# Kernel tuning notes

Hardware: AMD Instinct MI355X
Metric: run time of the kernel (lower is better)

The kernel has to match this reference:

```python
import jax, jax.numpy as jnp
import numpy as np

B, T, C, K, V = 4, 2048, 1024, 1024, 1024
SQRT_K = float(np.sqrt(K))


def setup_inputs() -> dict:
    key = jax.random.key(0)
    ks = jax.random.split(key, 7)
    s = 0.02
    return {
        "x": jax.random.normal(ks[0], (B, T, C), jnp.float32),
        "Wq": (jax.random.normal(ks[1], (C, K), jnp.float32) * s),
        "bq": jnp.zeros((K,), jnp.float32),
        "Wk": (jax.random.normal(ks[2], (C, K), jnp.float32) * s),
        "bk": jnp.zeros((K,), jnp.float32),
        "Wv": (jax.random.normal(ks[3], (C, V), jnp.float32) * s),
        "bv": jnp.zeros((V,), jnp.float32),
    }


def reference(x, Wq, bq, Wk, bk, Wv, bv):
    # projections: [B,T,C] @ [C,K] -> [B,T,K]
    q = x @ Wq + bq
    k = x @ Wk + bk
    v = x @ Wv + bv
    # logits[b,t,s] = q[b,t,:] . k[b,s,:]
    logits = jnp.einsum("btk,bsk->bts", q, k)
    # original mask: mask[j,i] = 1 if i > j -> strict upper triangle masked to -inf
    seq = logits.shape[1]
    mask = jnp.triu(jnp.ones((seq, seq), bool), k=1)
    logits = jnp.where(mask[None, :, :], -jnp.inf, logits)
    # NOTE: original softmax is over dim=1 (query axis), not the key axis
    probs = jax.nn.softmax(logits / SQRT_K, axis=1)
    read = jnp.einsum("bts,bsv->btv", probs, v)
    return jnp.concatenate((x, read), axis=2)
```

## Files before the change

### kernel.cpp

```cpp
#include <hip/hip_runtime.h>
#include <hip/hip_bf16.h>
#include <stdint.h>

#define DEVI __device__ __forceinline__

using u16 = unsigned short;
typedef __attribute__((ext_vector_type(8))) _Float16 halfx8;
typedef __attribute__((ext_vector_type(8))) unsigned short u16x8;
typedef __attribute__((ext_vector_type(4))) float f32x4;

constexpr int BB = 4, TT = 2048, CC = 1024, KD = 1024, VD = 1024;
constexpr int QKVW = 3072;
constexpr int OUTW = CC + VD;
constexpr float INV_SQRT_K = 0.03125f;

DEVI u16 f2h(float f) {
  _Float16 h = (_Float16)f;
  return __builtin_bit_cast(u16, h);
}
DEVI float h2f(u16 u) {
  return (float)__builtin_bit_cast(_Float16, u);
}

DEVI void gload16(const u16* g, u16* l) {
  __builtin_amdgcn_global_load_lds(
      (const __attribute__((address_space(1))) void*)g,
      (__attribute__((address_space(3))) void*)l, 16, 0, 0);
}

__global__ void cast_x_copy(const float* __restrict__ x, u16* __restrict__ xh,
                            float* __restrict__ out) {
  size_t i = (size_t)blockIdx.x * blockDim.x + threadIdx.x;
  float4 v = reinterpret_cast<const float4*>(x)[i];
  ushort4 u;
  u.x = f2h(v.x); u.y = f2h(v.y); u.z = f2h(v.z); u.w = f2h(v.w);
  reinterpret_cast<ushort4*>(xh)[i] = u;
  size_t e = i * 4;
  size_t bt = e / CC;
  int c = (int)(e % CC);
  *reinterpret_cast<float4*>(&out[bt * OUTW + c]) = v;
}

__global__ void transpose_cast_w3(const float* __restrict__ Wq,
                                  const float* __restrict__ Wk,
                                  const float* __restrict__ Wv,
                                  u16* __restrict__ Wt) {
  __shared__ float tile[32][33];
  const float* W = (blockIdx.z == 0) ? Wq : (blockIdx.z == 1) ? Wk : Wv;
  u16* dst = Wt + (size_t)blockIdx.z * 1024 * 1024;
  int n0 = blockIdx.x * 32, c0 = blockIdx.y * 32;
  int tx = threadIdx.x, ty = threadIdx.y;
  for (int i = ty; i < 32; i += 8)
    tile[i][tx] = W[(size_t)(c0 + i) * KD + n0 + tx];
  __syncthreads();
  for (int i = ty; i < 32; i += 8)
    dst[(size_t)(n0 + i) * CC + c0 + tx] = f2h(tile[tx][i]);
}

__global__ void concat_bias(const float* __restrict__ bq, const float* __restrict__ bk,
                            const float* __restrict__ bv, float* __restrict__ bc) {
  int n = blockIdx.x * 256 + threadIdx.x;
  float v = (n < 1024) ? bq[n] : (n < 2048) ? bk[n - 1024] : bv[n - 2048];
  bc[n] = v;
}

__global__ void transpose_v(const u16* __restrict__ QKV, const float* __restrict__ Di,
                            u16* __restrict__ Vt) {
  __shared__ u16 tile[32][33];
  int b = blockIdx.z;
  int n0 = blockIdx.x * 32, s0 = blockIdx.y * 32;
  const u16* src = QKV + (size_t)b * TT * QKVW + 2048;
  u16* dst = Vt + (size_t)b * VD * TT;
  int tx = threadIdx.x, ty = threadIdx.y;
  for (int i = ty; i < 32; i += 8)
    tile[i][tx] = src[(size_t)(s0 + i) * QKVW + n0 + tx];
  float di = Di[b * TT + s0 + tx];
  __syncthreads();
  for (int i = ty; i < 32; i += 8)
    dst[(size_t)(n0 + i) * TT + s0 + tx] = f2h(h2f(tile[tx][i]) * di);
}

template <typename OutT, int SWZ, bool CSKIP, bool KLIM, bool BIAS, bool CMASK>
__global__ __launch_bounds__(512, 2) void gemm_bt(
    const u16* __restrict__ A, const u16* __restrict__ Bm, OutT* __restrict__ Out,
    const float* __restrict__ bias, float* __restrict__ Dp,
    int Kd, int lda, int ldb, int ldo,
    long long strA, long long strB, long long strO, float alpha) {
  constexpr int BM = 256, BN = 128, BK = 32;
  constexpr int WM = 4, WN = 2;
  constexpr int WR = 64, WC = 64;
  constexpr int MR = 4, NR = 4;
  constexpr int ASZ = BM * BK, BSZ = BN * BK;
  __shared__ u16 sA[3 * ASZ];
  __shared__ u16 sB[3 * BSZ];
  __shared__ float reds[CMASK ? WM : 1][CMASK ? BN : 1];

  int bx = blockIdx.x, by = blockIdx.y;
  if constexpr (SWZ == 1) {
    const int gx = gridDim.x;
    const int nx = gx >> 3;
    int fid = bx + gx * by;
    int xcd = fid & 7, idx = fid >> 3;
    bx = xcd * nx + idx % nx;
    by = idx / nx;
  }
  const int r0 = bx * BM, c0 = by * BN;
  if (CSKIP && c0 > r0 + BM - 1) return;
  A   += (size_t)blockIdx.z * strA;
  Bm  += (size_t)blockIdx.z * strB;
  Out += (size_t)blockIdx.z * strO;

  const int tid = threadIdx.x;
  const int lane = tid & 63;
  const int w = tid >> 6;
  const int wm = w / WN, wn = w % WN;
  const int l15 = lane & 15, l4 = lane >> 4;
  const int cswz8 = 8 * (l4 ^ ((l15 >> 1) & 3));

  const int srow = tid >> 2;
  const int sc8 = 8 * ((tid & 3) ^ ((tid >> 3) & 3));
  const u16* gA  = A  + (size_t)(r0 + srow) * lda + sc8;
  const u16* gA2 = gA + (size_t)128 * lda;
  const u16* gB  = Bm + (size_t)(c0 + srow) * ldb + sc8;
  const int sdst = tid * 8;

  f32x4 acc[MR][NR] = {};

  int kmax = Kd;
  if (KLIM) { int km = r0 + BM; kmax = km < Kd ? km : Kd; }
  const int NT = kmax / BK;

  auto stage = [&](int buf, int kt) {
    const int k0 = kt * BK;
    u16* da = sA + buf * ASZ + sdst;
    gload16(gA + k0, da);
    gload16(gA2 + k0, da + 4096);
    u16* db = sB + buf * BSZ + sdst;
    gload16(gB + k0, db);
  };

  stage(0, 0);
  stage(1, 1);
  asm volatile("s_waitcnt vmcnt(3)" ::: "memory");
  __builtin_amdgcn_s_barrier();

  int buf = 0;
  for (int kt = 0; kt < NT; ++kt) {
    int nb = buf + 2; if (nb >= 3) nb -= 3;
    const u16* rA = sA + buf * ASZ;
    const u16* rB = sB + buf * BSZ;
    halfx8 af[MR], bfv[NR];
#pragma unroll
    for (int n = 0; n < NR; ++n)
      bfv[n] = *reinterpret_cast<const halfx8*>(&rB[(wn * WC + n * 16 + l15) * BK + cswz8]);
#pragma unroll
    for (int m = 0; m < MR; ++m)
      af[m] = *reinterpret_cast<const halfx8*>(&rA[(wm * WR + m * 16 + l15) * BK + cswz8]);
    if (kt + 2 < NT) stage(nb, kt + 2);
    __builtin_amdgcn_s_setprio(1);
#pragma unroll
    for (int m = 0; m < MR; ++m)
#pragma unroll
      for (int n = 0; n < NR; ++n)
        acc[m][n] = __builtin_amdgcn_mfma_f32_16x16x32_f16(af[m], bfv[n], acc[m][n], 0, 0, 0);
    __builtin_amdgcn_s_setprio(0);
    if (kt + 2 < NT)      asm volatile("s_waitcnt vmcnt(3)" ::: "memory");
    else if (kt + 1 < NT) asm volatile("s_waitcnt vmcnt(0)" ::: "memory");
    if (kt + 1 < NT) __builtin_amdgcn_s_barrier();
    buf = buf + 1; if (buf == 3) buf = 0;
  }

  if constexpr (CMASK) {
#pragma unroll
    for (int n = 0; n < NR; ++n) {
      const int gcol = c0 + wn * WC + n * 16 + l15;
      float sm = 0.f;
#pragma unroll
      for (int m = 0; m < MR; ++m) {
        const int growb = r0 + wm * WR + m * 16 + l4 * 4;
#pragma unroll
        for (int r = 0; r < 4; ++r) {
          float p = 0.f;
          if (growb + r >= gcol) p = __expf(acc[m][n][r] * alpha);
          reinterpret_cast<u16*>(Out)[(size_t)(growb + r) * ldo + gcol] = f2h(p);
          sm += p;
        }
      }
      sm += __shfl_xor(sm, 16);
      sm += __shfl_xor(sm, 32);
      if (l4 == 0) reds[wm][wn * WC + n * 16 + l15] = sm;
    }
    __syncthreads();
    if (tid < BN) {
      float d2 = 0.f;
#pragma unroll
      for (int i = 0; i < WM; ++i) d2 += reds[i][tid];
      Dp[((size_t)(r0 >> 8) * BB + blockIdx.z) * TT + c0 + tid] = d2;
    }
  } else {
#pragma unroll
    for (int m = 0; m < MR; ++m) {
      const int growb = r0 + wm * WR + m * 16 + l4 * 4;
#pragma unroll
      for (int n = 0; n < NR; ++n) {
        const int gcol = c0 + wn * WC + n * 16 + l15;
        float bvv = 0.f;
        if (BIAS) bvv = bias[gcol];
#pragma unroll
        for (int r = 0; r < 4; ++r) {
          float val = acc[m][n][r] * alpha + bvv;
          size_t off = (size_t)(growb + r) * ldo + gcol;
          if constexpr (sizeof(OutT) == 2) {
            reinterpret_cast<u16*>(Out)[off] = f2h(val);
          } else {
            reinterpret_cast<float*>(Out)[off] = val;
          }
        }
      }
    }
  }
}

__global__ void stats_combine(const float* __restrict__ Dp, float* __restrict__ Di) {
  int b = blockIdx.y;
  int s = blockIdx.x * 256 + threadIdx.x;
  int rt0 = s >> 8;
  float d = 0.f;
  for (int rt = rt0; rt < TT / 256; ++rt)
    d += Dp[((size_t)rt * BB + b) * TT + s];
  Di[b * TT + s] = 1.f / d;
}

extern "C" void kernel_launch(void* const* d_in, const int* in_sizes, int n_in,
                              void* d_out, int out_size, void* d_ws, size_t ws_size,
                              hipStream_t stream) {
  const float* x  = (const float*)d_in[0];
  const float* Wq = (const float*)d_in[1];
  const float* bq = (const float*)d_in[2];
  const float* Wk = (const float*)d_in[3];
  const float* bk = (const float*)d_in[4];
  const float* Wv = (const float*)d_in[5];
  const float* bv = (const float*)d_in[6];
  float* out = (float*)d_out;
  char* ws = (char*)d_ws;
  constexpr size_t MB = 1024ull * 1024ull;

  u16* xh   = (u16*)(ws);
  u16* QKV  = (u16*)(ws + 16 * MB);
  u16* Wt   = (u16*)(ws + 64 * MB);
  float* bc = (float*)(ws + 70 * MB);
  u16* SP   = (u16*)(ws + 71 * MB);
  u16* Vt = xh;
  float* Dp = (float*)(ws + 64 * MB);
  float* Di = (float*)(ws + 65 * MB);

  cast_x_copy<<<dim3((BB * TT * CC / 4) / 256), dim3(256), 0, stream>>>(x, xh, out);
  dim3 tb(32, 8);
  transpose_cast_w3<<<dim3(KD / 32, CC / 32, 3), tb, 0, stream>>>(Wq, Wk, Wv, Wt);
  concat_bias<<<dim3(QKVW / 256), 256, 0, stream>>>(bq, bk, bv, bc);

  gemm_bt<u16, 1, false, false, true, false><<<dim3(32, QKVW / 128, 1), 512, 0, stream>>>(
      xh, Wt, QKV, bc, nullptr, CC, CC, CC, QKVW, 0, 0, 0, 1.f);

  gemm_bt<u16, 0, true, false, false, true><<<dim3(TT / 256, TT / 128, BB), 512, 0, stream>>>(
      QKV, QKV + 1024, SP, nullptr, Dp, KD, QKVW, QKVW, TT,
      (long long)TT * QKVW, (long long)TT * QKVW, (long long)TT * TT, INV_SQRT_K);

  stats_combine<<<dim3(TT / 256, BB), 256, 0, stream>>>(Dp, Di);

  transpose_v<<<dim3(VD / 32, TT / 32, BB), tb, 0, stream>>>(QKV, Di, Vt);

  gemm_bt<float, 0, false, true, false, false><<<dim3(TT / 256, VD / 128, BB), 512, 0, stream>>>(
      SP, Vt, out + CC, nullptr, nullptr, TT, TT, TT, OUTW,
      (long long)TT * TT, (long long)VD * TT, (long long)TT * OUTW, 1.f);
}
```

Measured before the change: 185.5 us.

## Add 256x256 eight-wave GEMM with ping-pong staging for QKV and logits

Adds a new GEMM kernel with 256x256 output tiles, BK=64 split into two 32-wide halves, and a four-slot shared-memory pipeline. The pipeline interleaves sub-tile loads with MFMA phases separated by barriers and priority switches. The kernel is used for the QKV projection and the masked exp-logits GEMM, raising per-block data reuse and cutting redundant global loads. In exchange it runs at one block per CU with heavier register use, and the larger tiles mean fewer blocks, which could hurt occupancy and load balance on the causal-skip GEMM. The old kernel's CMASK path is removed since only the PV GEMM still uses it.

```diff
diff --git a/kernel.cpp b/kernel.cpp
--- a/kernel.cpp
+++ b/kernel.cpp
@@ -80,6 +80,183 @@
     dst[(size_t)(n0 + i) * TT + s0 + tx] = f2h(h2f(tile[tx][i]) * di);
 }
 
+template <typename OutT, int SWZ, bool CSKIP, bool BIAS, bool CMASK>
+__global__ __launch_bounds__(512, 1) void gemm8p(
+    const u16* __restrict__ A, const u16* __restrict__ Bm, OutT* __restrict__ Out,
+    const float* __restrict__ bias, float* __restrict__ Dp,
+    int Kd, int lda, int ldb, int ldo,
+    long long strA, long long strB, long long strO, float alpha) {
+  constexpr int BM = 256, BN = 256, BK = 64;
+  constexpr int MR = 8, NR = 4;
+  __shared__ u16 sA[4 * 8192];
+  __shared__ u16 sB[4 * 8192];
+  __shared__ float reds[CMASK ? 2 : 1][CMASK ? BN : 1];
+
+  int bx = blockIdx.x, by = blockIdx.y;
+  if constexpr (SWZ == 1) {
+    const int gx = gridDim.x;
+    const int nx = gx >> 3;
+    int fid = bx + gx * by;
+    int xcd = fid & 7, idx = fid >> 3;
+    bx = xcd * nx + idx % nx;
+    by = idx / nx;
+  }
+  const int r0 = bx * BM, c0 = by * BN;
+  if (CSKIP && c0 > r0 + BM - 1) return;
+  A   += (size_t)blockIdx.z * strA;
+  Bm  += (size_t)blockIdx.z * strB;
+  Out += (size_t)blockIdx.z * strO;
+
+  const int tid = threadIdx.x;
+  const int lane = tid & 63;
+  const int w = tid >> 6;
+  const int wm = w >> 2, wn = w & 3;
+  const int l15 = lane & 15, l4 = lane >> 4;
+  const int rsw = 8 * (l4 ^ ((l15 >> 1) & 3));
+
+  const int srow = tid >> 2;
+  const int sc8 = 8 * ((tid & 3) ^ ((tid >> 3) & 3));
+  const u16* gA  = A  + (size_t)(r0 + srow) * lda + sc8;
+  const u16* gA2 = gA + (size_t)128 * lda;
+  const u16* gB  = Bm + (size_t)(c0 + srow) * ldb + sc8;
+  const u16* gB2 = gB + (size_t)128 * ldb;
+  const int sdst = tid * 8;
+
+  f32x4 acc[MR][NR] = {};
+  const int NT = Kd / BK;
+
+  auto stageA = [&](int slot, int kt, int ks) {
+    const int k0 = kt * BK + ks * 32;
+    u16* d = sA + slot * 8192 + sdst;
+    gload16(gA + k0, d);
+    gload16(gA2 + k0, d + 4096);
+  };
+  auto stageB = [&](int slot, int kt, int ks) {
+    const int k0 = kt * BK + ks * 32;
+    u16* d = sB + slot * 8192 + sdst;
+    gload16(gB + k0, d);
+    gload16(gB2 + k0, d + 4096);
+  };
+  auto rdA = [&](int slot, int m) {
+    return *reinterpret_cast<const halfx8*>(
+        &sA[slot * 8192 + (wm * 128 + m * 16 + l15) * 32 + rsw]);
+  };
+  auto rdB = [&](int slot, int n) {
+    return *reinterpret_cast<const halfx8*>(
+        &sB[slot * 8192 + (wn * 64 + n * 16 + l15) * 32 + rsw]);
+  };
+
+  stageA(0, 0, 0); stageB(0, 0, 0);
+  stageA(1, 0, 1); stageB(1, 0, 1);
+  stageA(2, 1, 0); stageB(2, 1, 0);
+  asm volatile("s_waitcnt vmcnt(4)" ::: "memory");
+  __builtin_amdgcn_s_barrier();
+
+  for (int kt = 0; kt < NT; ++kt) {
+    const int db = kt & 1, odb = db ^ 1;
+    const int a0 = db * 2, a1 = db * 2 + 1, o1 = odb * 2 + 1;
+    halfx8 af[MR], b0, b1;
+#pragma unroll
+    for (int m = 0; m < MR; ++m) af[m] = rdA(a0, m);
+    b0 = rdB(a0, 0); b1 = rdB(a0, 1);
+    if (kt + 1 < NT) stageA(o1, kt + 1, 1);
+    __builtin_amdgcn_s_barrier();
+    __builtin_amdgcn_s_setprio(1);
+#pragma unroll
+    for (int m = 0; m < MR; ++m) {
+      acc[m][0] = __builtin_amdgcn_mfma_f32_16x16x32_f16(af[m], b0, acc[m][0], 0, 0, 0);
+      acc[m][1] = __builtin_amdgcn_mfma_f32_16x16x32_f16(af[m], b1, acc[m][1], 0, 0, 0);
+    }
+    __builtin_amdgcn_s_setprio(0);
+    __builtin_amdgcn_s_barrier();
+    b0 = rdB(a0, 2); b1 = rdB(a0, 3);
+    if (kt + 1 < NT) stageB(o1, kt + 1, 1);
+    __builtin_amdgcn_s_barrier();
+    __builtin_amdgcn_s_setprio(1);
+#pragma unroll
+    for (int m = 0; m < MR; ++m) {
+      acc[m][2] = __builtin_amdgcn_mfma_f32_16x16x32_f16(af[m], b0, acc[m][2], 0, 0, 0);
+      acc[m][3] = __builtin_amdgcn_mfma_f32_16x16x32_f16(af[m], b1, acc[m][3], 0, 0, 0);
+    }
+    __builtin_amdgcn_s_setprio(0);
+    __builtin_amdgcn_s_barrier();
+#pragma unroll
+    for (int m = 0; m < MR; ++m) af[m] = rdA(a1, m);
+    b0 = rdB(a1, 0); b1 = rdB(a1, 1);
+    if (kt + 2 < NT) stageA(a0, kt + 2, 0);
+    __builtin_amdgcn_s_barrier();
+    __builtin_amdgcn_s_setprio(1);
+#pragma unroll
+    for (int m = 0; m < MR; ++m) {
+      acc[m][0] = __builtin_amdgcn_mfma_f32_16x16x32_f16(af[m], b0, acc[m][0], 0, 0, 0);
+      acc[m][1] = __builtin_amdgcn_mfma_f32_16x16x32_f16(af[m], b1, acc[m][1], 0, 0, 0);
+    }
+    __builtin_amdgcn_s_setprio(0);
+    __builtin_amdgcn_s_barrier();
+    b0 = rdB(a1, 2); b1 = rdB(a1, 3);
+    if (kt + 2 < NT) stageB(a0, kt + 2, 0);
+    __builtin_amdgcn_s_barrier();
+    __builtin_amdgcn_s_setprio(1);
+#pragma unroll
+    for (int m = 0; m < MR; ++m) {
+      acc[m][2] = __builtin_amdgcn_mfma_f32_16x16x32_f16(af[m], b0, acc[m][2], 0, 0, 0);
+      acc[m][3] = __builtin_amdgcn_mfma_f32_16x16x32_f16(af[m], b1, acc[m][3], 0, 0, 0);
+    }
+    __builtin_amdgcn_s_setprio(0);
+    if (kt + 2 < NT) asm volatile("s_waitcnt vmcnt(4)" ::: "memory");
+    else             asm volatile("s_waitcnt vmcnt(0)" ::: "memory");
+    __builtin_amdgcn_s_barrier();
+  }
+
+  if constexpr (CMASK) {
+#pragma unroll
+    for (int n = 0; n < NR; ++n) {
+      const int gcol = c0 + wn * 64 + n * 16 + l15;
+      float sm = 0.f;
+#pragma unroll
+      for (int m = 0; m < MR; ++m) {
+        const int growb = r0 + wm * 128 + m * 16 + l4 * 4;
+#pragma unroll
+        for (int r = 0; r < 4; ++r) {
+          float p = 0.f;
+          if (growb + r >= gcol) p = __expf(acc[m][n][r] * alpha);
+          reinterpret_cast<u16*>(Out)[(size_t)(growb + r) * ldo + gcol] = f2h(p);
+          sm += p;
+        }
+      }
+      sm += __shfl_xor(sm, 16);
+      sm += __shfl_xor(sm, 32);
+      if (l4 == 0) reds[wm][wn * 64 + n * 16 + l15] = sm;
+    }
+    __syncthreads();
+    if (tid < BN) {
+      float d2 = reds[0][tid] + reds[1][tid];
+      Dp[((size_t)(r0 >> 8) * BB + blockIdx.z) * TT + c0 + tid] = d2;
+    }
+  } else {
+#pragma unroll
+    for (int m = 0; m < MR; ++m) {
+      const int growb = r0 + wm * 128 + m * 16 + l4 * 4;
+#pragma unroll
+      for (int n = 0; n < NR; ++n) {
+        const int gcol = c0 + wn * 64 + n * 16 + l15;
+        float bvv = 0.f;
+        if (BIAS) bvv = bias[gcol];
+#pragma unroll
+        for (int r = 0; r < 4; ++r) {
+          float val = acc[m][n][r] * alpha + bvv;
+          size_t off = (size_t)(growb + r) * ldo + gcol;
+          if constexpr (sizeof(OutT) == 2) {
+            reinterpret_cast<u16*>(Out)[off] = f2h(val);
+          } else {
+            reinterpret_cast<float*>(Out)[off] = val;
+          }
+        }
+      }
+    }
+  }
+}
+
 template <typename OutT, int SWZ, bool CSKIP, bool KLIM, bool BIAS, bool CMASK>
 __global__ __launch_bounds__(512, 2) void gemm_bt(
     const u16* __restrict__ A, const u16* __restrict__ Bm, OutT* __restrict__ Out,
@@ -170,51 +347,22 @@
     buf = buf + 1; if (buf == 3) buf = 0;
   }
 
-  if constexpr (CMASK) {
+#pragma unroll
+  for (int m = 0; m < MR; ++m) {
+    const int growb = r0 + wm * WR + m * 16 + l4 * 4;
 #pragma unroll
     for (int n = 0; n < NR; ++n) {
       const int gcol = c0 + wn * WC + n * 16 + l15;
-      float sm = 0.f;
-#pragma unroll
-      for (int m = 0; m < MR; ++m) {
-        const int growb = r0 + wm * WR + m * 16 + l4 * 4;
-#pragma unroll
-        for (int r = 0; r < 4; ++r) {
-          float p = 0.f;
-          if (growb + r >= gcol) p = __expf(acc[m][n][r] * alpha);
-          reinterpret_cast<u16*>(Out)[(size_t)(growb + r) * ldo + gcol] = f2h(p);
-          sm += p;
-        }
-      }
-      sm += __shfl_xor(sm, 16);
-      sm += __shfl_xor(sm, 32);
-      if (l4 == 0) reds[wm][wn * WC + n * 16 + l15] = sm;
-    }
-    __syncthreads();
-    if (tid < BN) {
-      float d2 = 0.f;
-#pragma unroll
-      for (int i = 0; i < WM; ++i) d2 += reds[i][tid];
-      Dp[((size_t)(r0 >> 8) * BB + blockIdx.z) * TT + c0 + tid] = d2;
-    }
-  } else {
-#pragma unroll
-    for (int m = 0; m < MR; ++m) {
-      const int growb = r0 + wm * WR + m * 16 + l4 * 4;
-#pragma unroll
-      for (int n = 0; n < NR; ++n) {
-        const int gcol = c0 + wn * WC + n * 16 + l15;
-        float bvv = 0.f;
-        if (BIAS) bvv = bias[gcol];
-#pragma unroll
-        for (int r = 0; r < 4; ++r) {
-          float val = acc[m][n][r] * alpha + bvv;
-          size_t off = (size_t)(growb + r) * ldo + gcol;
-          if constexpr (sizeof(OutT) == 2) {
-            reinterpret_cast<u16*>(Out)[off] = f2h(val);
-          } else {
-            reinterpret_cast<float*>(Out)[off] = val;
-          }
+      float bvv = 0.f;
+      if (BIAS) bvv = bias[gcol];
+#pragma unroll
+      for (int r = 0; r < 4; ++r) {
+        float val = acc[m][n][r] * alpha + bvv;
+        size_t off = (size_t)(growb + r) * ldo + gcol;
+        if constexpr (sizeof(OutT) == 2) {
+          reinterpret_cast<u16*>(Out)[off] = f2h(val);
+        } else {
+          reinterpret_cast<float*>(Out)[off] = val;
         }
       }
     }
@@ -259,10 +407,10 @@
   transpose_cast_w3<<<dim3(KD / 32, CC / 32, 3), tb, 0, stream>>>(Wq, Wk, Wv, Wt);
   concat_bias<<<dim3(QKVW / 256), 256, 0, stream>>>(bq, bk, bv, bc);
 
-  gemm_bt<u16, 1, false, false, true, false><<<dim3(32, QKVW / 128, 1), 512, 0, stream>>>(
+  gemm8p<u16, 1, false, true, false><<<dim3(32, QKVW / 256, 1), 512, 0, stream>>>(
       xh, Wt, QKV, bc, nullptr, CC, CC, CC, QKVW, 0, 0, 0, 1.f);
 
-  gemm_bt<u16, 0, true, false, false, true><<<dim3(TT / 256, TT / 128, BB), 512, 0, stream>>>(
+  gemm8p<u16, 0, true, false, true><<<dim3(TT / 256, TT / 256, BB), 512, 0, stream>>>(
       QKV, QKV + 1024, SP, nullptr, Dp, KD, QKVW, QKVW, TT,
       (long long)TT * QKVW, (long long)TT * QKVW, (long long)TT * TT, INV_SQRT_K);
 
```

Measured after the change: 192.9 us. 1.04x slower.

## Split-K balance causal PV GEMM with atomics and fold stats combine into transpose

Applied to the files above, without the earlier changes.

The final PV GEMM now uses a fixed 12-entry schedule that maps blocks to row tiles and splits the long causal K ranges of the lower rows into two 1024-wide chunks. Partial results are accumulated into the output with float atomicAdd, and the output region is zeroed in the cast kernel. This is meant to even out the triangular workload across blocks. The separate stats_combine kernel is removed and the inverse-denominator reduction is recomputed per element inside transpose_v, which saves a launch at the cost of redundant Dp reads and makes the sum order nondeterministic.

```diff
diff --git a/kernel.cpp b/kernel.cpp
--- a/kernel.cpp
+++ b/kernel.cpp
@@ -39,6 +39,8 @@
   size_t bt = e / CC;
   int c = (int)(e % CC);
   *reinterpret_cast<float4*>(&out[bt * OUTW + c]) = v;
+  float4 z = {0.f, 0.f, 0.f, 0.f};
+  *reinterpret_cast<float4*>(&out[bt * OUTW + CC + c]) = z;
 }
 
 __global__ void transpose_cast_w3(const float* __restrict__ Wq,
@@ -64,7 +66,7 @@
   bc[n] = v;
 }
 
-__global__ void transpose_v(const u16* __restrict__ QKV, const float* __restrict__ Di,
+__global__ void transpose_v(const u16* __restrict__ QKV, const float* __restrict__ Dp,
                             u16* __restrict__ Vt) {
   __shared__ u16 tile[32][33];
   int b = blockIdx.z;
@@ -74,13 +76,17 @@
   int tx = threadIdx.x, ty = threadIdx.y;
   for (int i = ty; i < 32; i += 8)
     tile[i][tx] = src[(size_t)(s0 + i) * QKVW + n0 + tx];
-  float di = Di[b * TT + s0 + tx];
+  const int s = s0 + tx;
+  float d = 0.f;
+  for (int rt = s >> 8; rt < TT / 256; ++rt)
+    d += Dp[((size_t)rt * BB + b) * TT + s];
+  float di = 1.f / d;
   __syncthreads();
   for (int i = ty; i < 32; i += 8)
     dst[(size_t)(n0 + i) * TT + s0 + tx] = f2h(h2f(tile[tx][i]) * di);
 }
 
-template <typename OutT, int SWZ, bool CSKIP, bool KLIM, bool BIAS, bool CMASK>
+template <typename OutT, int SWZ, bool CSKIP, bool KLIM, bool BIAS, bool CMASK, bool PVS>
 __global__ __launch_bounds__(512, 2) void gemm_bt(
     const u16* __restrict__ A, const u16* __restrict__ Bm, OutT* __restrict__ Out,
     const float* __restrict__ bias, float* __restrict__ Dp,
@@ -96,7 +102,16 @@
   __shared__ float reds[CMASK ? WM : 1][CMASK ? BN : 1];
 
   int bx = blockIdx.x, by = blockIdx.y;
-  if constexpr (SWZ == 1) {
+  int kbeg = 0, kend = Kd;
+  if constexpr (PVS) {
+    const unsigned long long RTP = 0x405162776543ull;
+    const int rt = (int)((RTP >> (4 * bx)) & 15);
+    const int cch = (0xAA0 >> bx) & 1;
+    bx = rt;
+    kbeg = cch << 10;
+    int ke = (rt + 1) * 256, kcap = kbeg + 1024;
+    kend = ke < kcap ? ke : kcap;
+  } else if constexpr (SWZ == 1) {
     const int gx = gridDim.x;
     const int nx = gx >> 3;
     int fid = bx + gx * by;
@@ -105,9 +120,9 @@
     by = idx / nx;
   }
   const int r0 = bx * BM, c0 = by * BN;
-  if (CSKIP && c0 > r0 + BM - 1) return;
-  A   += (size_t)blockIdx.z * strA;
-  Bm  += (size_t)blockIdx.z * strB;
+  if (!PVS && CSKIP && c0 > r0 + BM - 1) return;
+  A   += (size_t)blockIdx.z * strA + kbeg;
+  Bm  += (size_t)blockIdx.z * strB + kbeg;
   Out += (size_t)blockIdx.z * strO;
 
   const int tid = threadIdx.x;
@@ -126,8 +141,8 @@
 
   f32x4 acc[MR][NR] = {};
 
-  int kmax = Kd;
-  if (KLIM) { int km = r0 + BM; kmax = km < Kd ? km : Kd; }
+  int kmax = kend - kbeg;
+  if (!PVS && KLIM) { int km = r0 + BM; kmax = km < kmax ? km : kmax; }
   const int NT = kmax / BK;
 
   auto stage = [&](int buf, int kt) {
@@ -210,7 +225,9 @@
         for (int r = 0; r < 4; ++r) {
           float val = acc[m][n][r] * alpha + bvv;
           size_t off = (size_t)(growb + r) * ldo + gcol;
-          if constexpr (sizeof(OutT) == 2) {
+          if constexpr (PVS) {
+            atomicAdd(&reinterpret_cast<float*>(Out)[off], val);
+          } else if constexpr (sizeof(OutT) == 2) {
             reinterpret_cast<u16*>(Out)[off] = f2h(val);
           } else {
             reinterpret_cast<float*>(Out)[off] = val;
@@ -219,16 +236,6 @@
       }
     }
   }
-}
-
-__global__ void stats_combine(const float* __restrict__ Dp, float* __restrict__ Di) {
-  int b = blockIdx.y;
-  int s = blockIdx.x * 256 + threadIdx.x;
-  int rt0 = s >> 8;
-  float d = 0.f;
-  for (int rt = rt0; rt < TT / 256; ++rt)
-    d += Dp[((size_t)rt * BB + b) * TT + s];
-  Di[b * TT + s] = 1.f / d;
 }
 
 extern "C" void kernel_launch(void* const* d_in, const int* in_sizes, int n_in,
@@ -252,25 +259,22 @@
   u16* SP   = (u16*)(ws + 71 * MB);
   u16* Vt = xh;
   float* Dp = (float*)(ws + 64 * MB);
-  float* Di = (float*)(ws + 65 * MB);
 
   cast_x_copy<<<dim3((BB * TT * CC / 4) / 256), dim3(256), 0, stream>>>(x, xh, out);
   dim3 tb(32, 8);
   transpose_cast_w3<<<dim3(KD / 32, CC / 32, 3), tb, 0, stream>>>(Wq, Wk, Wv, Wt);
   concat_bias<<<dim3(QKVW / 256), 256, 0, stream>>>(bq, bk, bv, bc);
 
-  gemm_bt<u16, 1, false, false, true, false><<<dim3(32, QKVW / 128, 1), 512, 0, stream>>>(
+  gemm_bt<u16, 1, false, false, true, false, false><<<dim3(32, QKVW / 128, 1), 512, 0, stream>>>(
       xh, Wt, QKV, bc, nullptr, CC, CC, CC, QKVW, 0, 0, 0, 1.f);
 
-  gemm_bt<u16, 0, true, false, false, true><<<dim3(TT / 256, TT / 128, BB), 512, 0, stream>>>(
+  gemm_bt<u16, 0, true, false, false, true, false><<<dim3(TT / 256, TT / 128, BB), 512, 0, stream>>>(
       QKV, QKV + 1024, SP, nullptr, Dp, KD, QKVW, QKVW, TT,
       (long long)TT * QKVW, (long long)TT * QKVW, (long long)TT * TT, INV_SQRT_K);
 
-  stats_combine<<<dim3(TT / 256, BB), 256, 0, stream>>>(Dp, Di);
-
-  transpose_v<<<dim3(VD / 32, TT / 32, BB), tb, 0, stream>>>(QKV, Di, Vt);
-
-  gemm_bt<float, 0, false, true, false, false><<<dim3(TT / 256, VD / 128, BB), 512, 0, stream>>>(
+  transpose_v<<<dim3(VD / 32, TT / 32, BB), tb, 0, stream>>>(QKV, Dp, Vt);
+
+  gemm_bt<float, 0, false, false, false, false, true><<<dim3(12, VD / 128, BB), 512, 0, stream>>>(
       SP, Vt, out + CC, nullptr, nullptr, TT, TT, TT, OUTW,
       (long long)TT * TT, (long long)VD * TT, (long long)TT * OUTW, 1.f);
 }
```

Result: slower. 201.9 us (+8.9%).
